# Performance work log

Hardware: AMD Instinct MI355X
Metric: run time of the kernel (lower is better)

The kernel has to match this reference:

```python
import jax, jax.numpy as jnp
import numpy as np

NF = 512
HEADS = 8
DHEAD = 64


def _dwconv(x, w):
    # x: [b, c, H, W], w: [c, 1, 3, 3] depthwise (groups=c), stride 1, pad 1
    return jax.lax.conv_general_dilated(
        x, w, window_strides=(1, 1), padding='SAME',
        feature_group_count=x.shape[1],
        dimension_numbers=('NCHW', 'OIHW', 'NCHW'))


def setup_inputs() -> dict:
    key = jax.random.key(0)
    ks = jax.random.split(key, 9)
    b, h, w, c = 4, 128, 128, NF
    hd = HEADS * DHEAD
    s = 1.0 / np.sqrt(c)
    return {
        'x_in': jax.random.normal(ks[0], (b, h, w, c), dtype=jnp.float32),
        'Wq': jax.random.normal(ks[1], (c, hd), dtype=jnp.float32) * s,
        'Wk': jax.random.normal(ks[2], (c, hd), dtype=jnp.float32) * s,
        'Wv': jax.random.normal(ks[3], (c, hd), dtype=jnp.float32) * s,
        'rescale': jnp.ones((HEADS, 1, 1), dtype=jnp.float32),
        'Wp': jax.random.normal(ks[4], (hd, c), dtype=jnp.float32) * s,
        'bp': jnp.zeros((c,), dtype=jnp.float32),
        'conv1_w': jax.random.normal(ks[5], (c, 1, 3, 3), dtype=jnp.float32) * (1.0 / 3.0),
        'conv2_w': jax.random.normal(ks[6], (c, 1, 3, 3), dtype=jnp.float32) * (1.0 / 3.0),
    }


def reference(x_in, Wq, Wk, Wv, rescale, Wp, bp, conv1_w, conv2_w):
    b, h, w, c = x_in.shape
    n = h * w
    x = x_in.reshape(b, n, c)
    # projections -> [b, heads, d, n] (transposed channel attention)
    def proj_t(W):
        return (x @ W).reshape(b, n, HEADS, DHEAD).transpose(0, 2, 3, 1)
    q = proj_t(Wq)
    k = proj_t(Wk)
    v_inp = x @ Wv  # [b, n, heads*d], kept for positional branch
    v = v_inp.reshape(b, n, HEADS, DHEAD).transpose(0, 2, 3, 1)
    # L2-normalize along token dim (last axis)
    qn = q / jnp.linalg.norm(q, axis=-1, keepdims=True)
    kn = k / jnp.linalg.norm(k, axis=-1, keepdims=True)
    # small d x d channel attention: attn = k @ q^T
    attn = jnp.einsum('bhdn,bhen->bhde', kn, qn) * rescale
    attn = jax.nn.softmax(attn, axis=-1)
    xo = jnp.einsum('bhde,bhen->bhdn', attn, v)
    xo = xo.transpose(0, 3, 1, 2).reshape(b, n, HEADS * DHEAD)
    out_c = (xo @ Wp + bp).reshape(b, h, w, c)
    # depthwise-conv positional branch on v_inp reshaped to image layout
    vimg = v_inp.reshape(b, h, w, c).transpose(0, 3, 1, 2)  # [b,c,h,w]
    y = _dwconv(vimg, conv1_w)
    y = jax.nn.gelu(y, approximate=False)  # F.gelu default is exact erf
    y = _dwconv(y, conv2_w)
    out_p = y.transpose(0, 2, 3, 1)
    return out_c + out_p
```

## Files before the change

kernel.cpp:

```cpp
#include <hip/hip_runtime.h>
#include <hip/hip_bf16.h>

typedef __attribute__((ext_vector_type(4))) float f32x4;
typedef __attribute__((ext_vector_type(8))) short s16x8;

__device__ __forceinline__ unsigned short f2bf(float f) {
    __hip_bfloat16 h = __float2bfloat16(f);
    return __builtin_bit_cast(unsigned short, h);
}
__device__ __forceinline__ float bf2f(unsigned short u) {
    return __builtin_bit_cast(float, ((unsigned)u) << 16);
}
__device__ __forceinline__ float2 bfpair(unsigned u) {
    float2 r;
    r.x = __builtin_bit_cast(float, u << 16);
    r.y = __builtin_bit_cast(float, u & 0xffff0000u);
    return r;
}
__device__ __forceinline__ void gload_lds16(const void* g, void* l) {
    __builtin_amdgcn_global_load_lds(
        (const __attribute__((address_space(1))) void*)g,
        (__attribute__((address_space(3))) void*)l, 16, 0, 0);
}
__device__ __forceinline__ float gelu_tanh(float x) {
    const float y = 0.7978845608028654f * (x + 0.044715f * x * x * x);
    const float t = __expf(-2.f * fabsf(y));
    const float th = (1.f - t) / (1.f + t);
    return 0.5f * x * (1.f + copysignf(th, y));
}

__global__ __launch_bounds__(256)
void k_cvt_tr(const float* __restrict__ in, unsigned short* __restrict__ XBF,
              unsigned short* __restrict__ XT) {
    __shared__ __align__(16) unsigned short tile[64 * 64];
    const int t  = threadIdx.x;
    const int c0 = blockIdx.x * 64;
    const int ty = blockIdx.y;
    const long tokg = (long)ty * 64;
    const int cq = t & 15, r0 = t >> 4;
#pragma unroll
    for (int p = 0; p < 4; ++p) {
        const int tok = r0 + p * 16;
        const float4 v = *(const float4*)(in + (tokg + tok) * 512 + c0 + cq * 4);
        union { unsigned short h[4]; uint2 u; } pk;
        pk.h[0] = f2bf(v.x); pk.h[1] = f2bf(v.y); pk.h[2] = f2bf(v.z); pk.h[3] = f2bf(v.w);
        *(uint2*)(XBF + (tokg + tok) * 512 + c0 + cq * 4) = pk.u;
        const int T = tok >> 3, i = tok & 7;
#pragma unroll
        for (int j = 0; j < 4; ++j) {
            const int c = cq * 4 + j;
            tile[c * 64 + ((T ^ (c & 7)) * 8 + i)] = pk.h[j];
        }
    }
    __syncthreads();
    const int b  = ty >> 8;
    const long tb = (long)(ty & 255) * 64;
    const int T2 = t & 7;
#pragma unroll
    for (int q = 0; q < 2; ++q) {
        const int c = (t >> 3) + q * 32;
        const uint4 v = *(const uint4*)&tile[c * 64 + ((T2 ^ (c & 7)) * 8)];
        *(uint4*)(XT + ((long)(b * 512 + c0 + c)) * 16384 + tb + T2 * 8) = v;
    }
}

__global__ __launch_bounds__(256)
void k_build_wcat(const float* __restrict__ Wq, const float* __restrict__ Wk,
                  const float* __restrict__ Wv, const float* __restrict__ Wp,
                  unsigned short* __restrict__ WcatT) {
    __shared__ float t[32][33];
    const int k0 = blockIdx.x * 32;
    const int j0 = blockIdx.y * 32;
    const float* src = (j0 < 512) ? Wq : (j0 < 1024 ? Wk : (j0 < 1536 ? Wv : Wp));
    const int jc0 = j0 & 511;
    const int r = threadIdx.x >> 5, c = threadIdx.x & 31;
#pragma unroll
    for (int rr = 0; rr < 4; ++rr) {
        const int k = k0 + r + rr * 8;
        t[c][r + rr * 8] = src[(long)k * 512 + jc0 + c];
    }
    __syncthreads();
#pragma unroll
    for (int rr = 0; rr < 4; ++rr) {
        const int j = j0 + r + rr * 8;
        WcatT[(long)j * 512 + k0 + c] = f2bf(t[r + rr * 8][c]);
    }
}

#define BM 128
#define BN 128
#define BK 64

template<int OUT_BF16, int BIAS, int ADDC>
__global__ __launch_bounds__(256, 2)
void gemm_mfma(const unsigned short* __restrict__ A, const unsigned short* __restrict__ B,
               void* __restrict__ C_, const float* __restrict__ bias,
               const unsigned short* __restrict__ addc,
               int lda, int ldb, int ldc, int K, long sA, long sB, long sC) {
    __shared__ __align__(16) unsigned short As[BM * BK];
    __shared__ __align__(16) unsigned short Bs[BN * BK];
    const int tid  = threadIdx.x;
    const int wave = tid >> 6;
    const int lane = tid & 63;
    const int wm = wave >> 1, wn = wave & 1;
    const int bm0 = blockIdx.y * BM;
    const int bn0 = blockIdx.x * BN;
    const long bz = blockIdx.z;
    A += bz * sA;
    B += bz * sB;

    const int l15 = lane & 15;
    const int l4  = lane >> 4;

    f32x4 acc[4][4];
#pragma unroll
    for (int i = 0; i < 4; ++i)
#pragma unroll
        for (int j = 0; j < 4; ++j) acc[i][j] = (f32x4){0.f, 0.f, 0.f, 0.f};

    const int srow    = wave * 8 + (lane >> 3);
    const int schunk0 = lane & 7;
    const int arow_b  = wm * 64 + l15;
    const int brow_b  = wn * 64 + l15;

    const int nk = K / BK;
    for (int kt = 0; kt < nk; ++kt) {
        const int k0 = kt * BK;
#pragma unroll
        for (int i = 0; i < 4; ++i) {
            const int r  = i * 32 + srow;
            const int gc = schunk0 ^ (r & 7);
            gload_lds16(A + (long)(bm0 + r) * lda + (k0 + gc * 8), &As[(i * 32 + wave * 8) * BK]);
            gload_lds16(B + (long)(bn0 + r) * ldb + (k0 + gc * 8), &Bs[(i * 32 + wave * 8) * BK]);
        }
        __syncthreads();
        s16x8 af[4][2], bfr[4][2];
#pragma unroll
        for (int mi = 0; mi < 4; ++mi) {
            const int row = arow_b + mi * 16;
#pragma unroll
            for (int ki = 0; ki < 2; ++ki) {
                const int ch = (ki * 4 + l4) ^ (row & 7);
                af[mi][ki] = *(const s16x8*)&As[row * BK + ch * 8];
            }
        }
#pragma unroll
        for (int ni = 0; ni < 4; ++ni) {
            const int row = brow_b + ni * 16;
#pragma unroll
            for (int ki = 0; ki < 2; ++ki) {
                const int ch = (ki * 4 + l4) ^ (row & 7);
                bfr[ni][ki] = *(const s16x8*)&Bs[row * BK + ch * 8];
            }
        }
#pragma unroll
        for (int ki = 0; ki < 2; ++ki)
#pragma unroll
            for (int mi = 0; mi < 4; ++mi)
#pragma unroll
                for (int ni = 0; ni < 4; ++ni)
                    acc[mi][ni] = __builtin_amdgcn_mfma_f32_16x16x32_bf16(
                        af[mi][ki], bfr[ni][ki], acc[mi][ni], 0, 0, 0);
        __syncthreads();
    }

#pragma unroll
    for (int mi = 0; mi < 4; ++mi) {
        const int row0 = bm0 + wm * 64 + mi * 16 + l4 * 4;
#pragma unroll
        for (int ni = 0; ni < 4; ++ni) {
            const int col = bn0 + wn * 64 + ni * 16 + l15;
            if (OUT_BF16) {
                unsigned short* C = (unsigned short*)C_ + bz * sC;
#pragma unroll
                for (int j = 0; j < 4; ++j)
                    C[(long)(row0 + j) * ldc + col] = f2bf(acc[mi][ni][j]);
            } else {
                float* C = (float*)C_ + bz * sC;
                const float bv = BIAS ? bias[col] : 0.f;
#pragma unroll
                for (int j = 0; j < 4; ++j) {
                    float v = acc[mi][ni][j] + bv;
                    if (ADDC) v += bf2f(addc[bz * sC + (long)(row0 + j) * ldc + col]);
                    C[(long)(row0 + j) * ldc + col] = v;
                }
            }
        }
    }
}

__global__ __launch_bounds__(256, 2)
void gemm_gram(const unsigned short* __restrict__ XT, float* __restrict__ P) {
    __shared__ __align__(16) unsigned short As[128 * 64];
    __shared__ __align__(16) unsigned short Bs[128 * 64];
    const int tid = threadIdx.x, wave = tid >> 6, lane = tid & 63;
    const int wm = wave >> 1, wn = wave & 1;
    const int bm0 = blockIdx.y * 128, bn0 = blockIdx.x * 128;
    const int z = blockIdx.z, b = z >> 3, chunk = z & 7;
    const unsigned short* A = XT + (long)b * 512 * 16384;
    const int l15 = lane & 15, l4 = lane >> 4;

    f32x4 acc[4][4];
#pragma unroll
    for (int i = 0; i < 4; ++i)
#pragma unroll
        for (int j = 0; j < 4; ++j) acc[i][j] = (f32x4){0.f, 0.f, 0.f, 0.f};

    const int srow = wave * 8 + (lane >> 3);
    const int sch  = lane & 7;
    const int arow_b = wm * 64 + l15;
    const int brow_b = wn * 64 + l15;

    for (int kt = 0; kt < 32; ++kt) {
        const long k0 = (long)chunk * 2048 + kt * 64;
#pragma unroll
        for (int i = 0; i < 4; ++i) {
            const int r  = i * 32 + srow;
            const int gc = sch ^ (r & 7);
            gload_lds16(A + (long)(bm0 + r) * 16384 + k0 + gc * 8, &As[(i * 32 + wave * 8) * 64]);
            gload_lds16(A + (long)(bn0 + r) * 16384 + k0 + gc * 8, &Bs[(i * 32 + wave * 8) * 64]);
        }
        __syncthreads();
        s16x8 af[4][2], bfr[4][2];
#pragma unroll
        for (int mi = 0; mi < 4; ++mi) {
            const int row = arow_b + mi * 16;
#pragma unroll
            for (int ki = 0; ki < 2; ++ki)
                af[mi][ki] = *(const s16x8*)&As[row * 64 + (((ki * 4 + l4) ^ (row & 7))) * 8];
        }
#pragma unroll
        for (int ni = 0; ni < 4; ++ni) {
            const int row = brow_b + ni * 16;
#pragma unroll
            for (int ki = 0; ki < 2; ++ki)
                bfr[ni][ki] = *(const s16x8*)&Bs[row * 64 + (((ki * 4 + l4) ^ (row & 7))) * 8];
        }
#pragma unroll
        for (int ki = 0; ki < 2; ++ki)
#pragma unroll
            for (int mi = 0; mi < 4; ++mi)
#pragma unroll
                for (int ni = 0; ni < 4; ++ni)
                    acc[mi][ni] = __builtin_amdgcn_mfma_f32_16x16x32_bf16(
                        af[mi][ki], bfr[ni][ki], acc[mi][ni], 0, 0, 0);
        __syncthreads();
    }

    float* Pb = P + ((long)((b * 8 + chunk) * 16 + blockIdx.y * 4 + blockIdx.x)) * 16384;
#pragma unroll
    for (int mi = 0; mi < 4; ++mi) {
        const int row0 = wm * 64 + mi * 16 + l4 * 4;
#pragma unroll
        for (int ni = 0; ni < 4; ++ni) {
            const int col = wn * 64 + ni * 16 + l15;
#pragma unroll
            for (int j = 0; j < 4; ++j)
                Pb[(row0 + j) * 128 + col] = acc[mi][ni][j];
        }
    }
}

__global__ void k_greduce(const float* __restrict__ P, unsigned* __restrict__ GB2) {
    const long idx = (long)blockIdx.x * 256 + threadIdx.x;
    const int b   = (int)(idx >> 17);
    const int rem = (int)(idx & 131071);
    const int c   = rem >> 8;
    const int cp0 = (rem & 255) * 2;
    const int tp  = (c >> 7) * 4 + (cp0 >> 7);
    const int e   = (c & 127) * 128 + (cp0 & 127);
    const float* Pp = P + ((long)(b * 8) * 16 + tp) * 16384 + e;
    float s0 = 0.f, s1 = 0.f;
#pragma unroll
    for (int ch = 0; ch < 8; ++ch) {
        const float2 v = *(const float2*)(Pp + (long)ch * 16 * 16384);
        s0 += v.x; s1 += v.y;
    }
    GB2[idx] = (unsigned)f2bf(s0) | ((unsigned)f2bf(s1) << 16);
}

__global__ void k_ssq(const unsigned short* __restrict__ WCT, const unsigned short* __restrict__ T1e,
                      const unsigned short* __restrict__ T2e, float* __restrict__ SSQ) {
    const int b = blockIdx.y;
    const int o = blockIdx.x * 256 + threadIdx.x;
    const unsigned short* wrow;
    const unsigned short* trow;
    if (o < 512) {
        wrow = WCT + (long)o * 512;
        trow = T1e + (long)b * 262144 + (long)o * 512;
    } else {
        const int d = o - 512;
        wrow = WCT + 262144 + (long)d * 512;
        trow = T2e + (long)b * 262144 + (long)d * 512;
    }
    float s = 0.f;
    for (int c = 0; c < 512; c += 8) {
        const s16x8 w = *(const s16x8*)&wrow[c];
        const s16x8 v = *(const s16x8*)&trow[c];
#pragma unroll
        for (int j = 0; j < 8; ++j)
            s += bf2f((unsigned short)w[j]) * bf2f((unsigned short)v[j]);
    }
    SSQ[b * 1024 + o] = s;
}

__global__ __launch_bounds__(256)
void k_softmax_bd(const float* __restrict__ attn, const float* __restrict__ sumsq,
                  const float* __restrict__ rescale, unsigned short* __restrict__ MBD) {
    __shared__ unsigned short TD[64 * 68];
    const int bh = blockIdx.x;
    const int b = bh >> 3, h = bh & 7;
    const int wave = threadIdx.x >> 6, e = threadIdx.x & 63;
    const float rs   = rescale[h];
    const float invq = rsqrtf(sumsq[b * 1024 + h * 64 + e]);
#pragma unroll 4
    for (int i = 0; i < 16; ++i) {
        const int d = wave * 16 + i;
        const float invk = rsqrtf(sumsq[b * 1024 + 512 + h * 64 + d]);
        const float v = attn[((long)b * 512 + h * 64 + d) * 512 + h * 64 + e] * invk * invq * rs;
        float mx = v;
#pragma unroll
        for (int off = 32; off >= 1; off >>= 1) mx = fmaxf(mx, __shfl_xor(mx, off));
        const float l = __expf(v - mx);
        float s = l;
#pragma unroll
        for (int off = 32; off >= 1; off >>= 1) s += __shfl_xor(s, off);
        TD[e * 68 + d] = f2bf(l / s);
    }
    __syncthreads();
    const int er = threadIdx.x >> 2, dc = (threadIdx.x & 3) * 16;
    union { unsigned short h[16]; uint4 u[2]; } pk;
#pragma unroll
    for (int j = 0; j < 16; ++j) pk.h[j] = TD[er * 68 + dc + j];
    uint4* dst = (uint4*)(MBD + ((long)b * 512 + h * 64 + er) * 512 + h * 64 + dc);
    dst[0] = pk.u[0];
    dst[1] = pk.u[1];
}

__global__ __launch_bounds__(256)
void k_conv1_gelu(const unsigned short* __restrict__ V,
                  const float* __restrict__ w, unsigned short* __restrict__ g) {
    const int x0 = blockIdx.x * 16;
    const int y  = blockIdx.y;
    const int b  = blockIdx.z;
    const int c0 = threadIdx.x * 2;
    float wq0[9], wq1[9];
#pragma unroll
    for (int i = 0; i < 9; ++i) { wq0[i] = w[c0 * 9 + i]; wq1[i] = w[(c0 + 1) * 9 + i]; }
    const long pixbase = (long)b * 16384;

    auto ld = [&](int yy, int xx) -> float2 {
        if (yy < 0 || yy > 127 || xx < 0 || xx > 127) return make_float2(0.f, 0.f);
        return bfpair(*(const unsigned*)(V + (pixbase + (long)yy * 128 + xx) * 512 + c0));
    };

    float2 col[3][6];
#pragma unroll
    for (int ky = 0; ky < 3; ++ky) {
        col[ky][0] = ld(y + ky - 1, x0 - 1);
        col[ky][1] = ld(y + ky - 1, x0);
    }
    for (int xq = 0; xq < 4; ++xq) {
        const int xb = x0 + xq * 4;
#pragma unroll
        for (int ky = 0; ky < 3; ++ky)
#pragma unroll
            for (int j = 0; j < 4; ++j)
                col[ky][2 + j] = ld(y + ky - 1, xb + 1 + j);
#pragma unroll
        for (int j = 0; j < 4; ++j) {
            float a0 = 0.f, a1 = 0.f;
#pragma unroll
            for (int ky = 0; ky < 3; ++ky)
#pragma unroll
                for (int kx = 0; kx < 3; ++kx) {
                    a0 += col[ky][j + kx].x * wq0[ky * 3 + kx];
                    a1 += col[ky][j + kx].y * wq1[ky * 3 + kx];
                }
            a0 = gelu_tanh(a0);
            a1 = gelu_tanh(a1);
            const unsigned up = (unsigned)f2bf(a0) | ((unsigned)f2bf(a1) << 16);
            *(unsigned*)(g + (pixbase + (long)y * 128 + xb + j) * 512 + c0) = up;
        }
#pragma unroll
        for (int ky = 0; ky < 3; ++ky) {
            col[ky][0] = col[ky][4];
            col[ky][1] = col[ky][5];
        }
    }
}

__global__ __launch_bounds__(256)
void k_conv2_bf(const unsigned short* __restrict__ gin,
                const float* __restrict__ w, unsigned short* __restrict__ outbf) {
    const int x0 = blockIdx.x * 16;
    const int y  = blockIdx.y;
    const int b  = blockIdx.z;
    const int c0 = threadIdx.x * 2;
    float wq0[9], wq1[9];
#pragma unroll
    for (int i = 0; i < 9; ++i) { wq0[i] = w[c0 * 9 + i]; wq1[i] = w[(c0 + 1) * 9 + i]; }
    const long pixbase = (long)b * 16384;

    auto ld = [&](int yy, int xx) -> float2 {
        if (yy < 0 || yy > 127 || xx < 0 || xx > 127) return make_float2(0.f, 0.f);
        return bfpair(*(const unsigned*)(gin + (pixbase + (long)yy * 128 + xx) * 512 + c0));
    };

    float2 col[3][6];
#pragma unroll
    for (int ky = 0; ky < 3; ++ky) {
        col[ky][0] = ld(y + ky - 1, x0 - 1);
        col[ky][1] = ld(y + ky - 1, x0);
    }
    for (int xq = 0; xq < 4; ++xq) {
        const int xb = x0 + xq * 4;
#pragma unroll
        for (int ky = 0; ky < 3; ++ky)
#pragma unroll
            for (int j = 0; j < 4; ++j)
                col[ky][2 + j] = ld(y + ky - 1, xb + 1 + j);
#pragma unroll
        for (int j = 0; j < 4; ++j) {
            float a0 = 0.f, a1 = 0.f;
#pragma unroll
            for (int ky = 0; ky < 3; ++ky)
#pragma unroll
                for (int kx = 0; kx < 3; ++kx) {
                    a0 += col[ky][j + kx].x * wq0[ky * 3 + kx];
                    a1 += col[ky][j + kx].y * wq1[ky * 3 + kx];
                }
            const unsigned up = (unsigned)f2bf(a0) | ((unsigned)f2bf(a1) << 16);
            *(unsigned*)(outbf + (pixbase + (long)y * 128 + xb + j) * 512 + c0) = up;
        }
#pragma unroll
        for (int ky = 0; ky < 3; ++ky) {
            col[ky][0] = col[ky][4];
            col[ky][1] = col[ky][5];
        }
    }
}

extern "C" void kernel_launch(void* const* d_in, const int* in_sizes, int n_in,
                              void* d_out, int out_size, void* d_ws, size_t ws_size,
                              hipStream_t stream) {
    const float* x_in    = (const float*)d_in[0];
    const float* Wq      = (const float*)d_in[1];
    const float* Wk      = (const float*)d_in[2];
    const float* Wv      = (const float*)d_in[3];
    const float* rescale = (const float*)d_in[4];
    const float* Wp      = (const float*)d_in[5];
    const float* bp      = (const float*)d_in[6];
    const float* c1w     = (const float*)d_in[7];
    const float* c2w     = (const float*)d_in[8];
    float* out = (float*)d_out;

    char* ws = (char*)d_ws;
    unsigned short* XBF = (unsigned short*)(ws);
    unsigned short* VBF = (unsigned short*)(ws + 67108864LL);
    unsigned short* XT  = (unsigned short*)(ws + 134217728LL);
    unsigned short* CV2 = XT;
    float*          P   = (float*)(ws + 201326592LL);
    unsigned short* WCT = (unsigned short*)(ws + 234881024LL);
    unsigned short* GB  = (unsigned short*)(ws + 236978176LL);
    unsigned short* T1e = (unsigned short*)(ws + 239075328LL);
    unsigned short* T2e = (unsigned short*)(ws + 241172480LL);
    float*          SSQ = (float*)(ws + 243269632LL);
    float*          ATTF= (float*)(ws + 243286016LL);
    unsigned short* MBD = (unsigned short*)(ws + 247480320LL);
    unsigned short* WEF = (unsigned short*)(ws + 249577472LL);

    (void)hipMemsetAsync(MBD, 0, 2097152, stream);

    k_cvt_tr<<<dim3(8, 1024), dim3(256), 0, stream>>>(x_in, XBF, XT);
    k_build_wcat<<<dim3(16, 64), dim3(256), 0, stream>>>(Wq, Wk, Wv, Wp, WCT);

    gemm_mfma<1, 0, 0><<<dim3(4, 512, 1), dim3(256), 0, stream>>>(
        XBF, WCT + 2 * 262144, (void*)VBF, nullptr, nullptr, 512, 512, 512, 512, 0L, 0L, 0L);

    gemm_gram<<<dim3(4, 4, 32), dim3(256), 0, stream>>>(XT, P);
    k_greduce<<<dim3(2048), dim3(256), 0, stream>>>(P, (unsigned*)GB);

    gemm_mfma<1, 0, 0><<<dim3(4, 4, 4), dim3(256), 0, stream>>>(
        WCT + 262144, GB, (void*)T2e, nullptr, nullptr, 512, 512, 512, 512, 0L, 262144L, 262144L);
    gemm_mfma<1, 0, 0><<<dim3(4, 4, 4), dim3(256), 0, stream>>>(
        WCT, GB, (void*)T1e, nullptr, nullptr, 512, 512, 512, 512, 0L, 262144L, 262144L);
    gemm_mfma<0, 0, 0><<<dim3(4, 4, 4), dim3(256), 0, stream>>>(
        T2e, WCT, (void*)ATTF, nullptr, nullptr, 512, 512, 512, 512, 262144L, 0L, 262144L);

    k_ssq<<<dim3(4, 4), dim3(256), 0, stream>>>(WCT, T1e, T2e, SSQ);
    k_softmax_bd<<<dim3(32), dim3(256), 0, stream>>>(ATTF, SSQ, rescale, MBD);

    gemm_mfma<1, 0, 0><<<dim3(4, 4, 4), dim3(256), 0, stream>>>(
        WCT + 3 * 262144, MBD, (void*)WEF, nullptr, nullptr, 512, 512, 512, 512, 0L, 262144L, 262144L);

    k_conv1_gelu<<<dim3(8, 128, 4), dim3(256), 0, stream>>>(VBF, c1w, XBF);
    k_conv2_bf<<<dim3(8, 128, 4), dim3(256), 0, stream>>>(XBF, c2w, CV2);

    gemm_mfma<0, 1, 1><<<dim3(4, 128, 4), dim3(256), 0, stream>>>(
        VBF, WEF, (void*)out, bp, CV2, 512, 512, 512, 512,
        (long)16384 * 512, 262144L, (long)16384 * 512);
}
```

Before: 395.5 us.

## Fuse depthwise convs via LDS halo tile, remap GEMM blocks, stage epilogue through LDS

```diff
diff --git a/kernel.cpp b/kernel.cpp
--- a/kernel.cpp
+++ b/kernel.cpp
@@ -97,15 +97,25 @@
                void* __restrict__ C_, const float* __restrict__ bias,
                const unsigned short* __restrict__ addc,
                int lda, int ldb, int ldc, int K, long sA, long sB, long sC) {
-    __shared__ __align__(16) unsigned short As[BM * BK];
-    __shared__ __align__(16) unsigned short Bs[BN * BK];
+    __shared__ __align__(16) unsigned short sm[BM * BK * 2];
+    unsigned short* As = sm;
+    unsigned short* Bs = sm + BM * BK;
+
     const int tid  = threadIdx.x;
     const int wave = tid >> 6;
     const int lane = tid & 63;
     const int wm = wave >> 1, wn = wave & 1;
-    const int bm0 = blockIdx.y * BM;
-    const int bn0 = blockIdx.x * BN;
-    const long bz = blockIdx.z;
+
+    const int nx = gridDim.x, ny = gridDim.y;
+    const int nwg = nx * ny * gridDim.z;
+    int lid = blockIdx.x + nx * (blockIdx.y + ny * blockIdx.z);
+    lid = (lid & 7) * (nwg >> 3) + (lid >> 3);
+    const int bxi = lid % nx;
+    const int rest = lid / nx;
+    const int byi = rest % ny;
+    const long bz = rest / ny;
+    const int bm0 = byi * BM;
+    const int bn0 = bxi * BN;
     A += bz * sA;
     B += bz * sB;
 
@@ -164,26 +174,67 @@
         __syncthreads();
     }
 
-#pragma unroll
-    for (int mi = 0; mi < 4; ++mi) {
-        const int row0 = bm0 + wm * 64 + mi * 16 + l4 * 4;
-#pragma unroll
-        for (int ni = 0; ni < 4; ++ni) {
-            const int col = bn0 + wn * 64 + ni * 16 + l15;
-            if (OUT_BF16) {
-                unsigned short* C = (unsigned short*)C_ + bz * sC;
-#pragma unroll
-                for (int j = 0; j < 4; ++j)
-                    C[(long)(row0 + j) * ldc + col] = f2bf(acc[mi][ni][j]);
-            } else {
-                float* C = (float*)C_ + bz * sC;
-                const float bv = BIAS ? bias[col] : 0.f;
-#pragma unroll
-                for (int j = 0; j < 4; ++j) {
-                    float v = acc[mi][ni][j] + bv;
-                    if (ADDC) v += bf2f(addc[bz * sC + (long)(row0 + j) * ldc + col]);
-                    C[(long)(row0 + j) * ldc + col] = v;
+    if (OUT_BF16) {
+        unsigned short* Cs = sm;
+        unsigned short* C = (unsigned short*)C_ + bz * sC;
+#pragma unroll
+        for (int pass = 0; pass < 2; ++pass) {
+            __syncthreads();
+            if (wn == pass) {
+#pragma unroll
+                for (int mi = 0; mi < 4; ++mi)
+#pragma unroll
+                    for (int ni = 0; ni < 4; ++ni)
+#pragma unroll
+                        for (int j = 0; j < 4; ++j)
+                            Cs[(wm * 64 + mi * 16 + l4 * 4 + j) * 64 + ni * 16 + l15] =
+                                f2bf(acc[mi][ni][j]);
+            }
+            __syncthreads();
+            const int colL = (tid & 7) * 8;
+#pragma unroll
+            for (int it = 0; it < 4; ++it) {
+                const int row = it * 32 + (tid >> 3);
+                const uint4 v = *(const uint4*)&Cs[row * 64 + colL];
+                *(uint4*)&C[(long)(bm0 + row) * ldc + bn0 + pass * 64 + colL] = v;
+            }
+        }
+    } else {
+        float* Cs = (float*)sm;
+        float* C = (float*)C_ + bz * sC;
+#pragma unroll
+        for (int pass = 0; pass < 2; ++pass) {
+            __syncthreads();
+            if (wn == pass) {
+#pragma unroll
+                for (int mi = 0; mi < 4; ++mi)
+#pragma unroll
+                    for (int ni = 0; ni < 4; ++ni)
+#pragma unroll
+                        for (int j = 0; j < 4; ++j)
+                            Cs[(wm * 64 + mi * 16 + l4 * 4 + j) * 64 + ni * 16 + l15] =
+                                acc[mi][ni][j];
+            }
+            __syncthreads();
+            const int colL = (tid & 15) * 4;
+#pragma unroll
+            for (int it = 0; it < 8; ++it) {
+                const int row = it * 16 + (tid >> 4);
+                f32x4 v = *(const f32x4*)&Cs[row * 64 + colL];
+                const long gr = bm0 + row;
+                const int gc = bn0 + pass * 64 + colL;
+                if (BIAS) {
+                    const float4 bv = *(const float4*)(bias + gc);
+                    v[0] += bv.x; v[1] += bv.y; v[2] += bv.z; v[3] += bv.w;
                 }
+                if (ADDC) {
+                    const uint2 a2 = *(const uint2*)(addc + bz * sC + gr * ldc + gc);
+                    v[0] += bf2f((unsigned short)(a2.x & 0xffff));
+                    v[1] += bf2f((unsigned short)(a2.x >> 16));
+                    v[2] += bf2f((unsigned short)(a2.y & 0xffff));
+                    v[3] += bf2f((unsigned short)(a2.y >> 16));
+                }
+                *(f32x4*)&C[gr * ldc + gc] = v;
             }
         }
     }
@@ -338,106 +389,62 @@
 }
 
 __global__ __launch_bounds__(256)
-void k_conv1_gelu(const unsigned short* __restrict__ V,
-                  const float* __restrict__ w, unsigned short* __restrict__ g) {
-    const int x0 = blockIdx.x * 16;
-    const int y  = blockIdx.y;
-    const int b  = blockIdx.z;
-    const int c0 = threadIdx.x * 2;
-    float wq0[9], wq1[9];
-#pragma unroll
-    for (int i = 0; i < 9; ++i) { wq0[i] = w[c0 * 9 + i]; wq1[i] = w[(c0 + 1) * 9 + i]; }
+void k_dwconv_fused(const unsigned short* __restrict__ V, const float* __restrict__ w1,
+                    const float* __restrict__ w2, unsigned short* __restrict__ outbf) {
+    __shared__ unsigned g[324 * 32];
+    const int t  = threadIdx.x;
+    const int cp = t & 31;
+    const int pq = t >> 5;
+    const int x0 = blockIdx.x * 16, y0 = blockIdx.y * 16;
+    const int zc = blockIdx.z;
+    const int b  = zc >> 3;
+    const int c0 = (zc & 7) * 64 + cp * 2;
     const long pixbase = (long)b * 16384;
 
-    auto ld = [&](int yy, int xx) -> float2 {
-        if (yy < 0 || yy > 127 || xx < 0 || xx > 127) return make_float2(0.f, 0.f);
-        return bfpair(*(const unsigned*)(V + (pixbase + (long)yy * 128 + xx) * 512 + c0));
-    };
-
-    float2 col[3][6];
-#pragma unroll
-    for (int ky = 0; ky < 3; ++ky) {
-        col[ky][0] = ld(y + ky - 1, x0 - 1);
-        col[ky][1] = ld(y + ky - 1, x0);
-    }
-    for (int xq = 0; xq < 4; ++xq) {
-        const int xb = x0 + xq * 4;
-#pragma unroll
-        for (int ky = 0; ky < 3; ++ky)
-#pragma unroll
-            for (int j = 0; j < 4; ++j)
-                col[ky][2 + j] = ld(y + ky - 1, xb + 1 + j);
-#pragma unroll
-        for (int j = 0; j < 4; ++j) {
+    float w1a[9], w1b[9], w2a[9], w2b[9];
+#pragma unroll
+    for (int i = 0; i < 9; ++i) {
+        w1a[i] = w1[c0 * 9 + i]; w1b[i] = w1[(c0 + 1) * 9 + i];
+        w2a[i] = w2[c0 * 9 + i]; w2b[i] = w2[(c0 + 1) * 9 + i];
+    }
+
+    for (int q = pq; q < 324; q += 8) {
+        const int gy = q / 18, gx = q - gy * 18;
+        const int yy = y0 + gy - 1, xx = x0 + gx - 1;
+        unsigned packed = 0;
+        if (yy >= 0 && yy < 128 && xx >= 0 && xx < 128) {
             float a0 = 0.f, a1 = 0.f;
 #pragma unroll
             for (int ky = 0; ky < 3; ++ky)
 #pragma unroll
                 for (int kx = 0; kx < 3; ++kx) {
-                    a0 += col[ky][j + kx].x * wq0[ky * 3 + kx];
-                    a1 += col[ky][j + kx].y * wq1[ky * 3 + kx];
+                    const int sy = yy + ky - 1, sx = xx + kx - 1;
+                    if (sy >= 0 && sy < 128 && sx >= 0 && sx < 128) {
+                        const float2 v = bfpair(*(const unsigned*)(V + (pixbase + (long)sy * 128 + sx) * 512 + c0));
+                        a0 += v.x * w1a[ky * 3 + kx];
+                        a1 += v.y * w1b[ky * 3 + kx];
+                    }
                 }
             a0 = gelu_tanh(a0);
             a1 = gelu_tanh(a1);
-            const unsigned up = (unsigned)f2bf(a0) | ((unsigned)f2bf(a1) << 16);
-            *(unsigned*)(g + (pixbase + (long)y * 128 + xb + j) * 512 + c0) = up;
-        }
-#pragma unroll
-        for (int ky = 0; ky < 3; ++ky) {
-            col[ky][0] = col[ky][4];
-            col[ky][1] = col[ky][5];
-        }
-    }
-}
-
-__global__ __launch_bounds__(256)
-void k_conv2_bf(const unsigned short* __restrict__ gin,
-                const float* __restrict__ w, unsigned short* __restrict__ outbf) {
-    const int x0 = blockIdx.x * 16;
-    const int y  = blockIdx.y;
-    const int b  = blockIdx.z;
-    const int c0 = threadIdx.x * 2;
-    float wq0[9], wq1[9];
-#pragma unroll
-    for (int i = 0; i < 9; ++i) { wq0[i] = w[c0 * 9 + i]; wq1[i] = w[(c0 + 1) * 9 + i]; }
-    const long pixbase = (long)b * 16384;
-
-    auto ld = [&](int yy, int xx) -> float2 {
-        if (yy < 0 || yy > 127 || xx < 0 || xx > 127) return make_float2(0.f, 0.f);
-        return bfpair(*(const unsigned*)(gin + (pixbase + (long)yy * 128 + xx) * 512 + c0));
-    };
-
-    float2 col[3][6];
-#pragma unroll
-    for (int ky = 0; ky < 3; ++ky) {
-        col[ky][0] = ld(y + ky - 1, x0 - 1);
-        col[ky][1] = ld(y + ky - 1, x0);
-    }
-    for (int xq = 0; xq < 4; ++xq) {
-        const int xb = x0 + xq * 4;
+            packed = (unsigned)f2bf(a0) | ((unsigned)f2bf(a1) << 16);
+        }
+        g[q * 32 + cp] = packed;
+    }
+    __syncthreads();
+    for (int q = pq; q < 256; q += 8) {
+        const int oy = q >> 4, ox = q & 15;
+        float a0 = 0.f, a1 = 0.f;
 #pragma unroll
         for (int ky = 0; ky < 3; ++ky)
 #pragma unroll
-            for (int j = 0; j < 4; ++j)
-                col[ky][2 + j] = ld(y + ky - 1, xb + 1 + j);
-#pragma unroll
-        for (int j = 0; j < 4; ++j) {
-            float a0 = 0.f, a1 = 0.f;
-#pragma unroll
-            for (int ky = 0; ky < 3; ++ky)
-#pragma unroll
-                for (int kx = 0; kx < 3; ++kx) {
-                    a0 += col[ky][j + kx].x * wq0[ky * 3 + kx];
-                    a1 += col[ky][j + kx].y * wq1[ky * 3 + kx];
-                }
-            const unsigned up = (unsigned)f2bf(a0) | ((unsigned)f2bf(a1) << 16);
-            *(unsigned*)(outbf + (pixbase + (long)y * 128 + xb + j) * 512 + c0) = up;
-        }
-#pragma unroll
-        for (int ky = 0; ky < 3; ++ky) {
-            col[ky][0] = col[ky][4];
-            col[ky][1] = col[ky][5];
-        }
+            for (int kx = 0; kx < 3; ++kx) {
+                const float2 v = bfpair(g[((oy + ky) * 18 + (ox + kx)) * 32 + cp]);
+                a0 += v.x * w2a[ky * 3 + kx];
+                a1 += v.y * w2b[ky * 3 + kx];
+            }
+        *(unsigned*)(outbf + (pixbase + (long)(y0 + oy) * 128 + x0 + ox) * 512 + c0) =
+            (unsigned)f2bf(a0) | ((unsigned)f2bf(a1) << 16);
     }
 }
 
@@ -494,8 +501,7 @@
     gemm_mfma<1, 0, 0><<<dim3(4, 4, 4), dim3(256), 0, stream>>>(
         WCT + 3 * 262144, MBD, (void*)WEF, nullptr, nullptr, 512, 512, 512, 512, 0L, 262144L, 262144L);
 
-    k_conv1_gelu<<<dim3(8, 128, 4), dim3(256), 0, stream>>>(VBF, c1w, XBF);
-    k_conv2_bf<<<dim3(8, 128, 4), dim3(256), 0, stream>>>(XBF, c2w, CV2);
+    k_dwconv_fused<<<dim3(8, 8, 32), dim3(256), 0, stream>>>(VBF, c1w, c2w, CV2);
 
     gemm_mfma<0, 1, 1><<<dim3(4, 128, 4), dim3(256), 0, stream>>>(
         VBF, WEF, (void*)out, bp, CV2, 512, 512, 512, 512,
```

Result: slower. 604.8 us (+52.9%).
